# Kernel optimization log

Measured on AMD Instinct MI355X. Metric: run time of the kernel, lower is better.

## Reference

```python
import jax, jax.numpy as jnp
import numpy as np

D_MODEL = 1024


def setup_inputs() -> dict:
    key = jax.random.key(0)
    ks = jax.random.split(key, 9)
    d = D_MODEL
    s = 1.0 / np.sqrt(d)
    return {
        "x": jax.random.normal(ks[0], (4, 2048, d), dtype=jnp.float32),
        "w_q": jax.random.normal(ks[1], (d, d), dtype=jnp.float32) * s,
        "b_q": jnp.zeros((d,), dtype=jnp.float32),
        "w_k": jax.random.normal(ks[2], (d, d), dtype=jnp.float32) * s,
        "b_k": jnp.zeros((d,), dtype=jnp.float32),
        "w_v": jax.random.normal(ks[3], (d, d), dtype=jnp.float32) * s,
        "b_v": jnp.zeros((d,), dtype=jnp.float32),
        "w_out": jax.random.normal(ks[4], (d, d), dtype=jnp.float32) * s,
        "b_out": jnp.zeros((d,), dtype=jnp.float32),
    }


def reference(x, w_q, b_q, w_k, b_k, w_v, b_v, w_out, b_out):
    d_model = x.shape[-1]
    # torch Linear: y = x @ W^T + b
    Q = jnp.einsum("bsd,ed->bse", x, w_q) + b_q
    K = jnp.einsum("bsd,ed->bse", x, w_k) + b_k
    V = jnp.einsum("bsd,ed->bse", x, w_v) + b_v
    scores = jnp.einsum("bqd,bkd->bqk", Q, K) / jnp.sqrt(jnp.float32(d_model)).astype(x.dtype)
    attn = jax.nn.softmax(scores, axis=-1)
    out = jnp.einsum("bqk,bkd->bqd", attn, V)
    return jnp.einsum("bsd,ed->bse", out, w_out) + b_out
```

## Files before the change

kernel.cpp:

```cpp
#include <hip/hip_runtime.h>


typedef __bf16 bf16x8 __attribute__((ext_vector_type(8)));
typedef float f32x4 __attribute__((ext_vector_type(4)));

__device__ __forceinline__ unsigned short f32_to_bf16(float f) {
  unsigned int u = __float_as_uint(f);
  u += 0x7fffu + ((u >> 16) & 1u);
  return (unsigned short)(u >> 16);
}

__device__ __forceinline__ void load_lds16(const void* g, void* l) {
  __builtin_amdgcn_global_load_lds(
      (const __attribute__((address_space(1))) void*)g,
      (__attribute__((address_space(3))) void*)l, 16, 0, 0);
}

__global__ __launch_bounds__(256) void cast_f32_bf16(
    const float4* __restrict__ in, ushort4* __restrict__ out, int n4) {
  int i = blockIdx.x * 256 + threadIdx.x;
  if (i < n4) {
    float4 f = in[i];
    ushort4 u;
    u.x = f32_to_bf16(f.x);
    u.y = f32_to_bf16(f.y);
    u.z = f32_to_bf16(f.z);
    u.w = f32_to_bf16(f.w);
    out[i] = u;
  }
}

__global__ __launch_bounds__(256) void gemm_bt(
    const unsigned short* __restrict__ A, const unsigned short* __restrict__ B,
    void* __restrict__ C, const float* __restrict__ bias,
    int M, int N, int K, float alpha, int out_bf16,
    long long sA, long long sB, long long sC) {
  __shared__ unsigned short As[128 * 64];
  __shared__ unsigned short Bs[128 * 64];

  const int bz = blockIdx.z;
  A += (long long)bz * sA;
  B += (long long)bz * sB;

  const int bm = blockIdx.y, bn = blockIdx.x;
  const int tid = threadIdx.x;
  const int lane = tid & 63, wave = tid >> 6;
  const int wr = wave >> 1, wc = wave & 1;
  const int l16 = lane & 15, quad = lane >> 4;

  f32x4 acc[4][4] = {};

  const int srow = tid >> 3;
  const int xr = srow & 7;
  const int scol = ((tid & 7) ^ xr) * 8;
  const unsigned short* gA = A + (long long)(bm * 128 + srow) * K + scol;
  const unsigned short* gB = B + (long long)(bn * 128 + srow) * K + scol;
  char* ldsA = (char*)As + wave * 1024;
  char* ldsB = (char*)Bs + wave * 1024;

  for (int k0 = 0; k0 < K; k0 += 64) {
#pragma unroll
    for (int r = 0; r < 4; r++)
      load_lds16(gA + k0 + (long long)r * 32 * K, ldsA + r * 4096);
#pragma unroll
    for (int r = 0; r < 4; r++)
      load_lds16(gB + k0 + (long long)r * 32 * K, ldsB + r * 4096);
    __syncthreads();

    const int swz = l16 & 7;
#pragma unroll
    for (int kk = 0; kk < 64; kk += 32) {
      bf16x8 af[4], bf[4];
      const int lc = (kk >> 3) + quad;
      const int pco = (lc ^ swz) * 8;
#pragma unroll
      for (int mi = 0; mi < 4; mi++)
        af[mi] = *(const bf16x8*)(As + (wr * 64 + mi * 16 + l16) * 64 + pco);
#pragma unroll
      for (int ni = 0; ni < 4; ni++)
        bf[ni] = *(const bf16x8*)(Bs + (wc * 64 + ni * 16 + l16) * 64 + pco);
#pragma unroll
      for (int mi = 0; mi < 4; mi++)
#pragma unroll
        for (int ni = 0; ni < 4; ni++)
          acc[mi][ni] = __builtin_amdgcn_mfma_f32_16x16x32_bf16(
              af[mi], bf[ni], acc[mi][ni], 0, 0, 0);
    }
    __syncthreads();
  }

  const int orow0 = bm * 128 + wr * 64 + quad * 4;
  const int ocol0 = bn * 128 + wc * 64 + l16;
  if (out_bf16) {
    unsigned short* Cp = (unsigned short*)C + (long long)bz * sC;
#pragma unroll
    for (int mi = 0; mi < 4; mi++)
#pragma unroll
      for (int ni = 0; ni < 4; ni++) {
        const int col = ocol0 + ni * 16;
        const float bv = bias ? bias[col] : 0.f;
#pragma unroll
        for (int r = 0; r < 4; r++) {
          const float o = acc[mi][ni][r] * alpha + bv;
          Cp[(long long)(orow0 + mi * 16 + r) * N + col] = f32_to_bf16(o);
        }
      }
  } else {
    float* Cp = (float*)C + (long long)bz * sC;
#pragma unroll
    for (int mi = 0; mi < 4; mi++)
#pragma unroll
      for (int ni = 0; ni < 4; ni++) {
        const int col = ocol0 + ni * 16;
        const float bv = bias ? bias[col] : 0.f;
#pragma unroll
        for (int r = 0; r < 4; r++) {
          const float o = acc[mi][ni][r] * alpha + bv;
          Cp[(long long)(orow0 + mi * 16 + r) * N + col] = o;
        }
      }
  }
}

__global__ __launch_bounds__(256) void transpose_v(
    const unsigned short* __restrict__ V, unsigned short* __restrict__ VT) {
  __shared__ unsigned short tile[64][65];
  const int d0 = blockIdx.x * 64, s0 = blockIdx.y * 64, b = blockIdx.z;
  const int t = threadIdx.x;
  const unsigned short* src = V + ((long long)b * 2048 + s0) * 1024 + d0;
#pragma unroll
  for (int i = 0; i < 16; i++) {
    int lin = t + i * 256;
    int r = lin >> 6, c = lin & 63;
    tile[r][c] = src[(long long)r * 1024 + c];
  }
  __syncthreads();
  unsigned short* dst = VT + ((long long)b * 1024 + d0) * 2048 + s0;
#pragma unroll
  for (int i = 0; i < 16; i++) {
    int lin = t + i * 256;
    int r = lin >> 6, c = lin & 63;
    dst[(long long)r * 2048 + c] = tile[c][r];
  }
}

__global__ __launch_bounds__(256) void softmax_rows(
    const float* __restrict__ S, unsigned short* __restrict__ P) {
  const long long row = blockIdx.x;
  const float* s = S + row * 2048;
  const int t = threadIdx.x;
  float v[8];
  float mx = -3.4e38f;
#pragma unroll
  for (int i = 0; i < 8; i++) {
    v[i] = s[t + i * 256];
    mx = fmaxf(mx, v[i]);
  }
#pragma unroll
  for (int o = 32; o >= 1; o >>= 1) mx = fmaxf(mx, __shfl_xor(mx, o));
  __shared__ float red[4], red2[4];
  if ((t & 63) == 0) red[t >> 6] = mx;
  __syncthreads();
  mx = fmaxf(fmaxf(red[0], red[1]), fmaxf(red[2], red[3]));
  float sum = 0.f;
#pragma unroll
  for (int i = 0; i < 8; i++) {
    v[i] = __expf(v[i] - mx);
    sum += v[i];
  }
#pragma unroll
  for (int o = 32; o >= 1; o >>= 1) sum += __shfl_xor(sum, o);
  if ((t & 63) == 0) red2[t >> 6] = sum;
  __syncthreads();
  sum = red2[0] + red2[1] + red2[2] + red2[3];
  const float inv = 1.0f / sum;
  unsigned short* p = P + row * 2048;
#pragma unroll
  for (int i = 0; i < 8; i++) p[t + i * 256] = f32_to_bf16(v[i] * inv);
}

extern "C" void kernel_launch(void* const* d_in, const int* in_sizes, int n_in,
                              void* d_out, int out_size, void* d_ws,
                              size_t ws_size, hipStream_t stream) {
  const float* x = (const float*)d_in[0];
  const float* wq = (const float*)d_in[1];
  const float* bq = (const float*)d_in[2];
  const float* wk = (const float*)d_in[3];
  const float* bk = (const float*)d_in[4];
  const float* wv = (const float*)d_in[5];
  const float* bv = (const float*)d_in[6];
  const float* wo = (const float*)d_in[7];
  const float* bo = (const float*)d_in[8];
  float* out = (float*)d_out;
  char* ws = (char*)d_ws;
  const size_t MB = 1ull << 20;

  unsigned short* xb  = (unsigned short*)(ws + 0);
  unsigned short* wqb = (unsigned short*)(ws + 16 * MB);
  unsigned short* wkb = (unsigned short*)(ws + 18 * MB);
  unsigned short* wvb = (unsigned short*)(ws + 20 * MB);
  unsigned short* wob = (unsigned short*)(ws + 22 * MB);
  unsigned short* Q   = (unsigned short*)(ws + 24 * MB);
  unsigned short* Kb  = (unsigned short*)(ws + 40 * MB);
  unsigned short* VT  = (unsigned short*)(ws + 56 * MB);
  unsigned short* V   = (unsigned short*)(ws + 72 * MB);
  float*          S   = (float*)(ws + 72 * MB);
  unsigned short* P   = Q;
  unsigned short* O   = xb;

  cast_f32_bf16<<<dim3(8192), dim3(256), 0, stream>>>((const float4*)x,
                                                      (ushort4*)xb, 2097152);
  cast_f32_bf16<<<dim3(1024), dim3(256), 0, stream>>>((const float4*)wq,
                                                      (ushort4*)wqb, 262144);
  cast_f32_bf16<<<dim3(1024), dim3(256), 0, stream>>>((const float4*)wk,
                                                      (ushort4*)wkb, 262144);
  cast_f32_bf16<<<dim3(1024), dim3(256), 0, stream>>>((const float4*)wv,
                                                      (ushort4*)wvb, 262144);
  cast_f32_bf16<<<dim3(1024), dim3(256), 0, stream>>>((const float4*)wo,
                                                      (ushort4*)wob, 262144);

  gemm_bt<<<dim3(8, 64, 1), dim3(256), 0, stream>>>(xb, wqb, Q, bq, 8192, 1024,
                                                    1024, 1.f, 1, 0, 0, 0);
  gemm_bt<<<dim3(8, 64, 1), dim3(256), 0, stream>>>(xb, wkb, Kb, bk, 8192, 1024,
                                                    1024, 1.f, 1, 0, 0, 0);
  gemm_bt<<<dim3(8, 64, 1), dim3(256), 0, stream>>>(xb, wvb, V, bv, 8192, 1024,
                                                    1024, 1.f, 1, 0, 0, 0);

  transpose_v<<<dim3(16, 32, 4), dim3(256), 0, stream>>>(V, VT);

  gemm_bt<<<dim3(16, 16, 4), dim3(256), 0, stream>>>(
      Q, Kb, S, nullptr, 2048, 2048, 1024, 0.03125f, 0, 2048ll * 1024,
      2048ll * 1024, 2048ll * 2048);

  softmax_rows<<<dim3(8192), dim3(256), 0, stream>>>(S, P);

  gemm_bt<<<dim3(8, 16, 4), dim3(256), 0, stream>>>(
      P, VT, O, nullptr, 2048, 1024, 2048, 1.f, 1, 2048ll * 2048, 1024ll * 2048,
      2048ll * 1024);

  gemm_bt<<<dim3(8, 64, 1), dim3(256), 0, stream>>>(O, wob, out, bo, 8192, 1024,
                                                    1024, 1.f, 0, 0, 0, 0);
}
```

Baseline: 344.6 us.

## Fuse QKV projections and switch GEMMs to 256x256 double-buffered pipelined kernel

Replaces the 128x128 single-buffered GEMM with a 256x256-tile, 512-thread kernel. It double-buffers LDS with half-tile staging interleaved between MFMA phases, using explicit waitcnt, barriers and setprio to overlap global loads with compute. The three Q/K/V projections are fused into one GEMM against contiguous concatenated weights and biases, with strided leading dimensions feeding the attention GEMMs directly. The larger tiles raise register and LDS pressure and leave fewer workgroups for the smaller batched GEMMs (128 blocks for P·V and the output projection), which may underfill the GPU.

```diff
diff --git a/kernel.cpp b/kernel.cpp
--- a/kernel.cpp
+++ b/kernel.cpp
@@ -30,13 +30,25 @@
   }
 }
 
-__global__ __launch_bounds__(256) void gemm_bt(
+__global__ __launch_bounds__(256) void concat3(
+    const float* __restrict__ a, const float* __restrict__ b,
+    const float* __restrict__ c, float* __restrict__ o) {
+  int i = blockIdx.x * 256 + threadIdx.x;
+  if (i < 1024)
+    o[i] = a[i];
+  else if (i < 2048)
+    o[i] = b[i - 1024];
+  else if (i < 3072)
+    o[i] = c[i - 2048];
+}
+
+__global__ __launch_bounds__(512, 2) void gemm_bt256(
     const unsigned short* __restrict__ A, const unsigned short* __restrict__ B,
     void* __restrict__ C, const float* __restrict__ bias,
-    int M, int N, int K, float alpha, int out_bf16,
+    int M, int N, int K, float alpha, int out_bf16, int lda, int ldb,
     long long sA, long long sB, long long sC) {
-  __shared__ unsigned short As[128 * 64];
-  __shared__ unsigned short Bs[128 * 64];
+  __shared__ unsigned short As[2][2][128][64];
+  __shared__ unsigned short Bs[2][2][128][64];
 
   const int bz = blockIdx.z;
   A += (long long)bz * sA;
@@ -45,94 +57,210 @@
   const int bm = blockIdx.y, bn = blockIdx.x;
   const int tid = threadIdx.x;
   const int lane = tid & 63, wave = tid >> 6;
-  const int wr = wave >> 1, wc = wave & 1;
+  const int wr = wave >> 2;
+  const int wc = wave & 3;
   const int l16 = lane & 15, quad = lane >> 4;
-
-  f32x4 acc[4][4] = {};
+  const int wbh = wc >> 1;
+  const int wbr = (wc & 1) * 64 + l16;
+  const int pc0 = (quad ^ (l16 & 7)) * 8;
+  const int pc1 = ((4 + quad) ^ (l16 & 7)) * 8;
 
   const int srow = tid >> 3;
-  const int xr = srow & 7;
-  const int scol = ((tid & 7) ^ xr) * 8;
-  const unsigned short* gA = A + (long long)(bm * 128 + srow) * K + scol;
-  const unsigned short* gB = B + (long long)(bn * 128 + srow) * K + scol;
-  char* ldsA = (char*)As + wave * 1024;
-  char* ldsB = (char*)Bs + wave * 1024;
-
-  for (int k0 = 0; k0 < K; k0 += 64) {
-#pragma unroll
-    for (int r = 0; r < 4; r++)
-      load_lds16(gA + k0 + (long long)r * 32 * K, ldsA + r * 4096);
-#pragma unroll
-    for (int r = 0; r < 4; r++)
-      load_lds16(gB + k0 + (long long)r * 32 * K, ldsB + r * 4096);
-    __syncthreads();
-
-    const int swz = l16 & 7;
-#pragma unroll
-    for (int kk = 0; kk < 64; kk += 32) {
-      bf16x8 af[4], bf[4];
-      const int lc = (kk >> 3) + quad;
-      const int pco = (lc ^ swz) * 8;
-#pragma unroll
-      for (int mi = 0; mi < 4; mi++)
-        af[mi] = *(const bf16x8*)(As + (wr * 64 + mi * 16 + l16) * 64 + pco);
-#pragma unroll
-      for (int ni = 0; ni < 4; ni++)
-        bf[ni] = *(const bf16x8*)(Bs + (wc * 64 + ni * 16 + l16) * 64 + pco);
-#pragma unroll
-      for (int mi = 0; mi < 4; mi++)
-#pragma unroll
-        for (int ni = 0; ni < 4; ni++)
-          acc[mi][ni] = __builtin_amdgcn_mfma_f32_16x16x32_bf16(
-              af[mi], bf[ni], acc[mi][ni], 0, 0, 0);
-    }
-    __syncthreads();
-  }
-
-  const int orow0 = bm * 128 + wr * 64 + quad * 4;
-  const int ocol0 = bn * 128 + wc * 64 + l16;
+  const int lch = (tid & 7) ^ (srow & 7);
+  const unsigned short* gA0 = A + (long long)(bm * 256 + srow) * lda + lch * 8;
+  const unsigned short* gB0 = B + (long long)(bn * 256 + srow) * ldb + lch * 8;
+
+  f32x4 acc[8][4] = {};
+  bf16x8 af[2][2];
+  bf16x8 bf[4][2];
+
+  const int NT = K >> 6;
+
+#define STAGE(GP, LB, BUF, H, KT, LD)                                       \
+  do {                                                                      \
+    const unsigned short* _s =                                              \
+        (GP) + (long long)(H) * 128 * (LD) + (KT) * 64;                     \
+    char* _d = (char*)(LB) + ((BUF) * 2 + (H)) * 16384 + wave * 1024;       \
+    load_lds16(_s, _d);                                                     \
+    load_lds16(_s + (long long)64 * (LD), _d + 8192);                       \
+  } while (0)
+
+#define DSA2(BUF, MIP)                                                      \
+  do {                                                                      \
+    _Pragma("unroll") for (int m2 = 0; m2 < 2; ++m2) {                      \
+      const unsigned short* _r =                                            \
+          &As[BUF][wr][(MIP) * 32 + m2 * 16 + l16][0];                      \
+      af[m2][0] = *(const bf16x8*)(_r + pc0);                               \
+      af[m2][1] = *(const bf16x8*)(_r + pc1);                               \
+    }                                                                       \
+  } while (0)
+
+#define DSB8(BUF)                                                           \
+  do {                                                                      \
+    _Pragma("unroll") for (int ni = 0; ni < 4; ++ni) {                      \
+      const unsigned short* _r = &Bs[BUF][wbh][wbr + ni * 16][0];           \
+      bf[ni][0] = *(const bf16x8*)(_r + pc0);                               \
+      bf[ni][1] = *(const bf16x8*)(_r + pc1);                               \
+    }                                                                       \
+  } while (0)
+
+#define MMP(MIP)                                                            \
+  do {                                                                      \
+    _Pragma("unroll") for (int m2 = 0; m2 < 2; ++m2)                        \
+        _Pragma("unroll") for (int ni = 0; ni < 4; ++ni) {                  \
+      f32x4* _a = &acc[(MIP) * 2 + m2][ni];                                 \
+      *_a = __builtin_amdgcn_mfma_f32_16x16x32_bf16(af[m2][0], bf[ni][0],   \
+                                                    *_a, 0, 0, 0);          \
+      *_a = __builtin_amdgcn_mfma_f32_16x16x32_bf16(af[m2][1], bf[ni][1],   \
+                                                    *_a, 0, 0, 0);          \
+    }                                                                       \
+  } while (0)
+
+#define BAR() __builtin_amdgcn_s_barrier()
+#define WLG() asm volatile("s_waitcnt lgkmcnt(0)" ::: "memory")
+#define WVM4() asm volatile("s_waitcnt vmcnt(4)" ::: "memory")
+#define P1() __builtin_amdgcn_s_setprio(1)
+#define P0() __builtin_amdgcn_s_setprio(0)
+
+  STAGE(gA0, As, 0, 0, 0, lda);
+  STAGE(gA0, As, 0, 1, 0, lda);
+  STAGE(gB0, Bs, 0, 0, 0, ldb);
+  STAGE(gB0, Bs, 0, 1, 0, ldb);
+  STAGE(gB0, Bs, 1, 0, 1, ldb);
+  STAGE(gB0, Bs, 1, 1, 1, ldb);
+  WVM4();
+  BAR();
+
+  for (int it = 0; it < (NT >> 1); ++it) {
+    const int t = 2 * it;
+    const int tn1 = t + 1;
+    const int tn2 = (t + 2 < NT) ? t + 2 : NT - 1;
+    const int tn3 = (t + 3 < NT) ? t + 3 : NT - 1;
+    DSB8(0);
+    DSA2(0, 0);
+    STAGE(gA0, As, 1, 0, tn1, lda);
+    BAR();
+    WLG();
+    P1();
+    MMP(0);
+    P0();
+    BAR();
+    DSA2(0, 1);
+    STAGE(gA0, As, 1, 1, tn1, lda);
+    BAR();
+    WLG();
+    P1();
+    MMP(1);
+    P0();
+    BAR();
+    DSA2(0, 2);
+    STAGE(gB0, Bs, 0, 0, tn2, ldb);
+    BAR();
+    WLG();
+    P1();
+    MMP(2);
+    P0();
+    BAR();
+    DSA2(0, 3);
+    STAGE(gB0, Bs, 0, 1, tn2, ldb);
+    BAR();
+    WLG();
+    P1();
+    MMP(3);
+    P0();
+    WVM4();
+    BAR();
+    DSB8(1);
+    DSA2(1, 0);
+    STAGE(gA0, As, 0, 0, tn2, lda);
+    BAR();
+    WLG();
+    P1();
+    MMP(0);
+    P0();
+    BAR();
+    DSA2(1, 1);
+    STAGE(gA0, As, 0, 1, tn2, lda);
+    BAR();
+    WLG();
+    P1();
+    MMP(1);
+    P0();
+    BAR();
+    DSA2(1, 2);
+    STAGE(gB0, Bs, 1, 0, tn3, ldb);
+    BAR();
+    WLG();
+    P1();
+    MMP(2);
+    P0();
+    BAR();
+    DSA2(1, 3);
+    STAGE(gB0, Bs, 1, 1, tn3, ldb);
+    BAR();
+    WLG();
+    P1();
+    MMP(3);
+    P0();
+    WVM4();
+    BAR();
+  }
+  asm volatile("s_waitcnt vmcnt(0)" ::: "memory");
+
+  const long long orow0 = (long long)bm * 256 + wr * 128 + quad * 4;
+  const int ocol0 = bn * 256 + wc * 64 + l16;
   if (out_bf16) {
     unsigned short* Cp = (unsigned short*)C + (long long)bz * sC;
 #pragma unroll
-    for (int mi = 0; mi < 4; mi++)
-#pragma unroll
-      for (int ni = 0; ni < 4; ni++) {
+    for (int mi = 0; mi < 8; ++mi)
+#pragma unroll
+      for (int ni = 0; ni < 4; ++ni) {
         const int col = ocol0 + ni * 16;
         const float bv = bias ? bias[col] : 0.f;
 #pragma unroll
-        for (int r = 0; r < 4; r++) {
+        for (int r = 0; r < 4; ++r) {
           const float o = acc[mi][ni][r] * alpha + bv;
-          Cp[(long long)(orow0 + mi * 16 + r) * N + col] = f32_to_bf16(o);
+          Cp[(orow0 + mi * 16 + r) * N + col] = f32_to_bf16(o);
         }
       }
   } else {
     float* Cp = (float*)C + (long long)bz * sC;
 #pragma unroll
-    for (int mi = 0; mi < 4; mi++)
-#pragma unroll
-      for (int ni = 0; ni < 4; ni++) {
+    for (int mi = 0; mi < 8; ++mi)
+#pragma unroll
+      for (int ni = 0; ni < 4; ++ni) {
         const int col = ocol0 + ni * 16;
         const float bv = bias ? bias[col] : 0.f;
 #pragma unroll
-        for (int r = 0; r < 4; r++) {
+        for (int r = 0; r < 4; ++r) {
           const float o = acc[mi][ni][r] * alpha + bv;
-          Cp[(long long)(orow0 + mi * 16 + r) * N + col] = o;
+          Cp[(orow0 + mi * 16 + r) * N + col] = o;
         }
       }
   }
+#undef STAGE
+#undef DSA2
+#undef DSB8
+#undef MMP
+#undef BAR
+#undef WLG
+#undef WVM4
+#undef P1
+#undef P0
 }
 
 __global__ __launch_bounds__(256) void transpose_v(
-    const unsigned short* __restrict__ V, unsigned short* __restrict__ VT) {
+    const unsigned short* __restrict__ V, unsigned short* __restrict__ VT,
+    int ldv) {
   __shared__ unsigned short tile[64][65];
   const int d0 = blockIdx.x * 64, s0 = blockIdx.y * 64, b = blockIdx.z;
   const int t = threadIdx.x;
-  const unsigned short* src = V + ((long long)b * 2048 + s0) * 1024 + d0;
+  const unsigned short* src = V + ((long long)b * 2048 + s0) * ldv + d0;
 #pragma unroll
   for (int i = 0; i < 16; i++) {
     int lin = t + i * 256;
     int r = lin >> 6, c = lin & 63;
-    tile[r][c] = src[(long long)r * 1024 + c];
+    tile[r][c] = src[(long long)r * ldv + c];
   }
   __syncthreads();
   unsigned short* dst = VT + ((long long)b * 1024 + d0) * 2048 + s0;
@@ -195,49 +323,45 @@
   char* ws = (char*)d_ws;
   const size_t MB = 1ull << 20;
 
-  unsigned short* xb  = (unsigned short*)(ws + 0);
-  unsigned short* wqb = (unsigned short*)(ws + 16 * MB);
-  unsigned short* wkb = (unsigned short*)(ws + 18 * MB);
-  unsigned short* wvb = (unsigned short*)(ws + 20 * MB);
-  unsigned short* wob = (unsigned short*)(ws + 22 * MB);
-  unsigned short* Q   = (unsigned short*)(ws + 24 * MB);
-  unsigned short* Kb  = (unsigned short*)(ws + 40 * MB);
-  unsigned short* VT  = (unsigned short*)(ws + 56 * MB);
-  unsigned short* V   = (unsigned short*)(ws + 72 * MB);
-  float*          S   = (float*)(ws + 72 * MB);
-  unsigned short* P   = Q;
-  unsigned short* O   = xb;
+  unsigned short* xb   = (unsigned short*)(ws + 0);
+  unsigned short* wqkv = (unsigned short*)(ws + 16 * MB);
+  unsigned short* wkb  = (unsigned short*)(ws + 18 * MB);
+  unsigned short* wvb  = (unsigned short*)(ws + 20 * MB);
+  unsigned short* wob  = (unsigned short*)(ws + 22 * MB);
+  unsigned short* QKV  = (unsigned short*)(ws + 24 * MB);
+  float*          S    = (float*)(ws + 72 * MB);
+  float*          bqkv = (float*)(ws + 72 * MB);
+  unsigned short* VT   = xb;
+  unsigned short* P    = QKV;
+  unsigned short* O    = (unsigned short*)(ws + 56 * MB);
 
   cast_f32_bf16<<<dim3(8192), dim3(256), 0, stream>>>((const float4*)x,
                                                       (ushort4*)xb, 2097152);
   cast_f32_bf16<<<dim3(1024), dim3(256), 0, stream>>>((const float4*)wq,
-                                                      (ushort4*)wqb, 262144);
+                                                      (ushort4*)wqkv, 262144);
   cast_f32_bf16<<<dim3(1024), dim3(256), 0, stream>>>((const float4*)wk,
                                                       (ushort4*)wkb, 262144);
   cast_f32_bf16<<<dim3(1024), dim3(256), 0, stream>>>((const float4*)wv,
                                                       (ushort4*)wvb, 262144);
   cast_f32_bf16<<<dim3(1024), dim3(256), 0, stream>>>((const float4*)wo,
                                                       (ushort4*)wob, 262144);
-
-  gemm_bt<<<dim3(8, 64, 1), dim3(256), 0, stream>>>(xb, wqb, Q, bq, 8192, 1024,
-                                                    1024, 1.f, 1, 0, 0, 0);
-  gemm_bt<<<dim3(8, 64, 1), dim3(256), 0, stream>>>(xb, wkb, Kb, bk, 8192, 1024,
-                                                    1024, 1.f, 1, 0, 0, 0);
-  gemm_bt<<<dim3(8, 64, 1), dim3(256), 0, stream>>>(xb, wvb, V, bv, 8192, 1024,
-                                                    1024, 1.f, 1, 0, 0, 0);
-
-  transpose_v<<<dim3(16, 32, 4), dim3(256), 0, stream>>>(V, VT);
-
-  gemm_bt<<<dim3(16, 16, 4), dim3(256), 0, stream>>>(
-      Q, Kb, S, nullptr, 2048, 2048, 1024, 0.03125f, 0, 2048ll * 1024,
-      2048ll * 1024, 2048ll * 2048);
+  concat3<<<dim3(12), dim3(256), 0, stream>>>(bq, bk, bv, bqkv);
+
+  gemm_bt256<<<dim3(12, 32, 1), dim3(512), 0, stream>>>(
+      xb, wqkv, QKV, bqkv, 8192, 3072, 1024, 1.f, 1, 1024, 1024, 0, 0, 0);
+
+  transpose_v<<<dim3(16, 32, 4), dim3(256), 0, stream>>>(QKV + 2048, VT, 3072);
+
+  gemm_bt256<<<dim3(8, 8, 4), dim3(512), 0, stream>>>(
+      QKV, QKV + 1024, S, nullptr, 2048, 2048, 1024, 0.03125f, 0, 3072, 3072,
+      2048ll * 3072, 2048ll * 3072, 2048ll * 2048);
 
   softmax_rows<<<dim3(8192), dim3(256), 0, stream>>>(S, P);
 
-  gemm_bt<<<dim3(8, 16, 4), dim3(256), 0, stream>>>(
-      P, VT, O, nullptr, 2048, 1024, 2048, 1.f, 1, 2048ll * 2048, 1024ll * 2048,
-      2048ll * 1024);
-
-  gemm_bt<<<dim3(8, 64, 1), dim3(256), 0, stream>>>(O, wob, out, bo, 8192, 1024,
-                                                    1024, 1.f, 0, 0, 0, 0);
-}
+  gemm_bt256<<<dim3(4, 8, 4), dim3(512), 0, stream>>>(
+      P, VT, O, nullptr, 2048, 1024, 2048, 1.f, 1, 2048, 2048, 2048ll * 2048,
+      1024ll * 2048, 2048ll * 1024);
+
+  gemm_bt256<<<dim3(4, 32, 1), dim3(512), 0, stream>>>(
+      O, wob, out, bo, 8192, 1024, 1024, 1.f, 0, 1024, 1024, 0, 0, 0);
+}
```

New measurement: 387.2 us. 12.4% more time.
